# Kernel tuning notes

Hardware: AMD Instinct MI355X
Metric: run time of the kernel (lower is better)

Reference implementation:

```python
import jax, jax.numpy as jnp
from jax import lax
import numpy as np

NUM_BLOCK, NUM_LAYER = 4, 10
DILATIONS = [2 ** (i % NUM_LAYER) for i in range(NUM_BLOCK * NUM_LAYER)]


def setup_inputs() -> dict:
    key = jax.random.key(0)
    ks = jax.random.split(key, 6)
    s = 0.05
    return {
        "x": jax.random.normal(ks[0], (8, 256, 16000), dtype=jnp.float32),
        "W_start": jax.random.normal(ks[1], (32, 256), dtype=jnp.float32) * s,
        "W_dil": jax.random.normal(ks[2], (40, 128, 32, 2), dtype=jnp.float32) * s,
        "W_res": jax.random.normal(ks[3], (40, 32, 128), dtype=jnp.float32) * s,
        "W_e1": jax.random.normal(ks[4], (256, 32), dtype=jnp.float32) * s,
        "W_e2": jax.random.normal(ks[5], (256, 256), dtype=jnp.float32) * s,
    }


def _causal_dilated_conv(x, w, dilation):
    # x: [B, Cin, T], w: [Cout, Cin, K=2]. Left-pad (K-1)*dilation -> causal,
    # equivalent to torch symmetric-pad-then-trim-right.
    pad = (w.shape[-1] - 1) * dilation
    return lax.conv_general_dilated(
        x, w, window_strides=(1,), padding=[(pad, 0)],
        rhs_dilation=(dilation,), dimension_numbers=("NCH", "OIH", "NCH"))


def reference(x, W_start, W_dil, W_res, W_e1, W_e2):
    # start 1x1 conv (no bias)
    residual = jnp.einsum("oc,bct->bot", W_start, x)  # [B,32,T]
    skips = jnp.zeros_like(residual)
    for i, d in enumerate(DILATIONS):
        h = _causal_dilated_conv(residual, W_dil[i], d)       # [B,128,T]
        g = jnp.tanh(h) * jax.nn.sigmoid(h)                   # gated activation
        skip = jnp.einsum("oc,bct->bot", W_res[i], g)         # 1x1 -> [B,32,T]
        residual = residual + skip
        skips = skips + skip
    h = jax.nn.relu(skips)
    h = jax.nn.relu(jnp.einsum("oc,bct->bot", W_e1, h))       # [B,256,T]
    logits = jnp.einsum("oc,bct->bot", W_e2, h)               # [B,256,T]
    return logits
```

## Files before the change

### kernel.cpp

```cpp
#include <hip/hip_runtime.h>
#include <math.h>

#define T_LEN 16000
#define NTILE 250
#define TT 64
#define NBLK 2000
#define LGRID 500

static const int N_RES = 8 * 32 * T_LEN;

typedef _Float16 half_t;
typedef __attribute__((ext_vector_type(8))) _Float16 halfx8;
typedef __attribute__((ext_vector_type(4))) _Float16 halfx4;
typedef __attribute__((ext_vector_type(16))) float f32x16;
typedef unsigned int uint32;
typedef unsigned short ushort16;

#define MFMA(a, b, c) __builtin_amdgcn_mfma_f32_32x32x16_f16((a), (b), (c), 0, 0, 0)

static __device__ inline uint32 packpair(float a, float b) {
  half_t ha = (half_t)a, hb = (half_t)b;
  return (uint32)__builtin_bit_cast(ushort16, ha) |
         ((uint32)__builtin_bit_cast(ushort16, hb) << 16);
}

__global__ __launch_bounds__(256) void repack_k(
    const float* __restrict__ Wd, const float* __restrict__ Wr,
    const float* __restrict__ Ws, const float* __restrict__ We1,
    const float* __restrict__ We2,
    half_t* __restrict__ WaG, half_t* __restrict__ WrG, half_t* __restrict__ WsS,
    half_t* __restrict__ We1S, half_t* __restrict__ We2S) {
  int i = blockIdx.x * 256 + threadIdx.x;
  if (i < 40 * 128 * 128) {
    int l = i >> 14, r = i & 16383, o = r >> 7, k = r & 127;
    int kk = k & 63, c = kk >> 1, s = kk & 1;
    float w = Wd[(((l * 128 + o) * 32 + c) << 1) + s];
    half_t w0 = (half_t)w;
    WaG[i] = (k < 64) ? w0 : (half_t)((w - (float)w0) * 2048.f);
  }
  if (i < 40 * 32 * 256) {
    int l = i >> 13, r = i & 8191, o2 = r >> 8, k = r & 255;
    int kk = k & 127;
    int ks = kk >> 4, lh = (kk >> 3) & 1, j = kk & 7;
    int mh = ks >> 2, til = (ks >> 1) & 1, ab = ks & 1;
    int m = mh * 64 + til * 32 + ab * 16 + (j & 3) + ((j >> 2) << 3) + lh * 4;
    float w = Wr[(l * 32 + o2) * 128 + m];
    half_t w0 = (half_t)w;
    WrG[i] = (k < 128) ? w0 : (half_t)((w - (float)w0) * 2048.f);
  }
  if (i < 16384) {
    int o = i >> 9, k = i & 511, kk = k & 255;
    int chan = (kk >> 1) + (kk & 1) * 128;
    float w = Ws[o * 256 + chan];
    half_t w0 = (half_t)w;
    WsS[i] = (k < 256) ? w0 : (half_t)((w - (float)w0) * 2048.f);
  }
  if (i < 16384) {
    int o = i >> 6, k = i & 63;
    float w = We1[o * 32 + (k & 31)];
    half_t w0 = (half_t)w;
    We1S[i] = (k < 32) ? w0 : (half_t)((w - (float)w0) * 2048.f);
  }
  if (i < 131072) {
    int o = i >> 9, k = i & 511;
    float w = We2[o * 256 + (k & 255)];
    half_t w0 = (half_t)w;
    We2S[i] = (k < 256) ? w0 : (half_t)((w - (float)w0) * 2048.f);
  }
}

__global__ __launch_bounds__(256, 2) void start_k(const float* __restrict__ x,
                                                  const half_t* __restrict__ WsS,
                                                  float* __restrict__ res) {
  __shared__ __align__(16) char sm[51200];
  const int XS_OFF = 0, SKB_OFF = 33792;
  int tid = threadIdx.x;
  int wave = tid >> 6, lane = tid & 63;
  int l31 = lane & 31, lhi = lane >> 5;
  int nh = wave & 1, kh = wave >> 1;
  int b = blockIdx.x / NTILE;
  int t0 = (blockIdx.x % NTILE) * TT;
  int cth = tid >> 3, twh = (tid & 7) * 8;

  f32x16 accH{}, accL{};
#pragma unroll
  for (int p = 0; p < 2; ++p) {
#pragma unroll
    for (int cc = 0; cc < 4; ++cc) {
      const float* p0 = x + ((size_t)b * 256 + cc * 32 + cth) * T_LEN + t0 + twh;
      const float* p1 = p0 + (size_t)128 * T_LEN;
      float u[8], v[8];
      *(float4*)u       = *(const float4*)p0;
      *(float4*)(u + 4) = *(const float4*)(p0 + 4);
      *(float4*)v       = *(const float4*)p1;
      *(float4*)(v + 4) = *(const float4*)(p1 + 4);
#pragma unroll
      for (int j = 0; j < 8; ++j) {
        int t = twh + j;
        int sw = ((t >> 3) & 3) << 5;
        uint32 pk;
        if (p == 0) {
          pk = packpair(u[j], v[j]);
        } else {
          float l0 = (u[j] - (float)(half_t)u[j]) * 2048.f;
          float l1 = (v[j] - (float)(half_t)v[j]) * 2048.f;
          pk = packpair(l0, l1);
        }
        *(uint32*)(sm + XS_OFF + t * 528 + (((cc * 32 + cth) * 4) ^ sw)) = pk;
      }
    }
    __syncthreads();
    {
      int colt = nh * 32 + l31;
      int sw = ((colt >> 3) & 3) << 5;
      const char* xr = sm + XS_OFF + colt * 528;
#pragma unroll
      for (int ks = 0; ks < 8; ++ks) {
        int kg = kh * 8 + ks;
        halfx8 bf = *(const halfx8*)(xr + ((kg * 32 + lhi * 16) ^ sw));
        halfx8 hiA = *(const halfx8*)(WsS + l31 * 512 + kg * 16 + lhi * 8);
        if (p == 0) {
          accH = MFMA(hiA, bf, accH);
          halfx8 loA = *(const halfx8*)(WsS + l31 * 512 + 256 + kg * 16 + lhi * 8);
          accL = MFMA(loA, bf, accL);
        } else {
          accL = MFMA(hiA, bf, accL);
        }
      }
    }
    __syncthreads();
  }
  {
    float* skb = (float*)(sm + SKB_OFF) + kh * 32 * 68;
#pragma unroll
    for (int r = 0; r < 16; ++r) {
      int row = (r & 3) + 8 * (r >> 2) + 4 * lhi;
      skb[row * 68 + nh * 32 + l31] = accH[r] + accL[r] * (1.f / 2048.f);
    }
  }
  __syncthreads();
  {
    const float* s0 = (const float*)(sm + SKB_OFF) + cth * 68 + twh;
    const float* s1 = s0 + 32 * 68;
    float* rp = res + ((size_t)b * 32 + cth) * T_LEN + t0 + twh;
#pragma unroll
    for (int vq = 0; vq < 8; vq += 4) {
      float4 sa = *(const float4*)(s0 + vq);
      float4 sb = *(const float4*)(s1 + vq);
      float4 o;
      o.x = sa.x + sb.x;
      o.y = sa.y + sb.y;
      o.z = sa.z + sb.z;
      o.w = sa.w + sb.w;
      *(float4*)(rp + vq) = o;
    }
  }
}

#define LOAD_TILE(TI, CV, PV)                                              \
  {                                                                        \
    int tl_ = blockIdx.x + (TI) * LGRID;                                   \
    int bb_ = tl_ / NTILE;                                                 \
    int tb_ = (tl_ - bb_ * NTILE) * TT;                                    \
    const float* rip_ = resIn + ((size_t)bb_ * 32 + cth) * T_LEN;          \
    *(float4*)(CV)       = *(const float4*)(rip_ + tb_ + twh);             \
    *(float4*)((CV) + 4) = *(const float4*)(rip_ + tb_ + twh + 4);         \
    int tp_ = tb_ + twh - d;                                               \
    if (tp_ >= 0 && (d & 3) == 0) {                                        \
      *(float4*)(PV)       = *(const float4*)(rip_ + tp_);                 \
      *(float4*)((PV) + 4) = *(const float4*)(rip_ + tp_ + 4);             \
    } else {                                                               \
      _Pragma("unroll")                                                    \
      for (int j_ = 0; j_ < 8; ++j_) {                                     \
        int q_ = tp_ + j_;                                                 \
        (PV)[j_] = (q_ >= 0) ? rip_[q_] : 0.f;                             \
      }                                                                    \
    }                                                                      \
  }

#define STAGE_TILE(CV, PV)                                                 \
  {                                                                        \
    _Pragma("unroll")                                                      \
    for (int j = 0; j < 8; ++j) {                                          \
      int t = twh + j;                                                     \
      int sw = ((t >> 3) & 3) << 5;                                        \
      char* zrow = sm + t * 272;                                           \
      half_t p0 = (half_t)(PV)[j];                                         \
      half_t c0 = (half_t)(CV)[j];                                         \
      float pl = ((PV)[j] - (float)p0) * 2048.f;                           \
      float cl = ((CV)[j] - (float)c0) * 2048.f;                           \
      *(uint32*)(zrow + ((cth * 4) ^ sw))       = packpair((PV)[j], (CV)[j]); \
      *(uint32*)(zrow + ((cth * 4 + 128) ^ sw)) = packpair(pl, cl);        \
    }                                                                      \
  }

#define TILE_BODY(TI, CV, PV, NCV, NPV, PREF)                                  \
  {                                                                            \
    int tile = blockIdx.x + (TI) * LGRID;                                      \
    int b = tile / NTILE;                                                      \
    int t0 = (tile - b * NTILE) * TT;                                          \
    if (PREF) { LOAD_TILE((TI) + 1, NCV, NPV); }                               \
                                      \
    f32x16 hi0{}, hi1{}, lo0{}, lo1{};                                         \
    {                                                                          \
      int colt = nh * 32 + l31;                                                \
      int sw = ((colt >> 3) & 3) << 5;                                         \
      const char* zr = sm + colt * 272;                                        \
      _Pragma("unroll")                                                        \
      for (int ks = 0; ks < 12; ++ks) {                                        \
        int brow = (ks < 4) ? ks * 16                                          \
                            : ((ks < 8) ? (ks & 3) * 16 + 64 : (ks & 3) * 16); \
        halfx8 bf = *(const halfx8*)(zr + ((brow * 2 + lhi * 16) ^ sw));       \
        if (ks < 4) {                                                          \
          hi0 = MFMA(a1h0[ks], bf, hi0);                                       \
          hi1 = MFMA(a1h1[ks], bf, hi1);                                       \
        } else if (ks < 8) {                                                   \
          lo0 = MFMA(a1h0[ks & 3], bf, lo0);                                   \
          lo1 = MFMA(a1h1[ks & 3], bf, lo1);                                   \
        } else {                                                               \
          lo0 = MFMA(a1l0[ks & 3], bf, lo0);                                   \
          lo1 = MFMA(a1l1[ks & 3], bf, lo1);                                   \
        }                                                                      \
      }                                                                        \
    }                                                                          \
                          \
    halfx8 gh0a, gh0b, gl0a, gl0b, gh1a, gh1b, gl1a, gl1b;                     \
    _Pragma("unroll")                                                          \
    for (int r = 0; r < 16; ++r) {                                             \
      float ha = hi0[r] + lo0[r] * (1.f / 2048.f);                             \
      float hb = hi1[r] + lo1[r] * (1.f / 2048.f);                             \
      ha = fmaxf(ha, -30.f);                                                   \
      hb = fmaxf(hb, -30.f);                                                   \
      float ea = __expf(-ha), eb = __expf(-hb);                                \
      float ga = (1.f - ea) * __builtin_amdgcn_rcpf(1.f + ea * ea);            \
      float gb = (1.f - eb) * __builtin_amdgcn_rcpf(1.f + eb * eb);            \
      half_t ga0 = (half_t)ga;                                                 \
      half_t gb0 = (half_t)gb;                                                 \
      half_t ga1 = (half_t)((ga - (float)ga0) * 2048.f);                       \
      half_t gb1 = (half_t)((gb - (float)gb0) * 2048.f);                       \
      if (r < 8) {                                                             \
        gh0a[r] = ga0; gl0a[r] = ga1; gh1a[r] = gb0; gl1a[r] = gb1;            \
      } else {                                                                 \
        gh0b[r - 8] = ga0; gl0b[r - 8] = ga1;                                  \
        gh1b[r - 8] = gb0; gl1b[r - 8] = gb1;                                  \
      }                                                                        \
    }                                                                          \
                         \
    f32x16 shi{}, slo{};                                                       \
    shi = MFMA(wrHi[0], gh0a, shi);                                            \
    shi = MFMA(wrHi[1], gh0b, shi);                                            \
    shi = MFMA(wrHi[2], gh1a, shi);                                            \
    shi = MFMA(wrHi[3], gh1b, shi);                                            \
    slo = MFMA(wrHi[0], gl0a, slo);                                            \
    slo = MFMA(wrHi[1], gl0b, slo);                                            \
    slo = MFMA(wrHi[2], gl1a, slo);                                            \
    slo = MFMA(wrHi[3], gl1b, slo);                                            \
    slo = MFMA(wrLo[0], gh0a, slo);                                            \
    slo = MFMA(wrLo[1], gh0b, slo);                                            \
    slo = MFMA(wrLo[2], gh1a, slo);                                            \
    slo = MFMA(wrLo[3], gh1b, slo);                                            \
                                      \
    {                                                                          \
      float* skb = (float*)(sm + SKB_OFF) + mh * 32 * 68;                      \
      _Pragma("unroll")                                                        \
      for (int r = 0; r < 16; ++r) {                                           \
        int row = (r & 3) + 8 * (r >> 2) + 4 * lhi;                            \
        skb[row * 68 + nh * 32 + l31] = shi[r] + slo[r] * (1.f / 2048.f);      \
      }                                                                        \
    }                                                                          \
    __syncthreads();                                                           \
                 \
    {                                                                          \
      const float* s0 = (const float*)(sm + SKB_OFF) + cth * 68 + twh;         \
      const float* s1 = s0 + 32 * 68;                                          \
      size_t base = ((size_t)b * 32 + cth) * T_LEN + t0 + twh;                 \
      _Pragma("unroll")                                                        \
      for (int v = 0; v < 8; v += 4) {                                         \
        float4 sa = *(const float4*)(s0 + v);                                  \
        float4 sb = *(const float4*)(s1 + v);                                  \
        float4 o;                                                              \
        o.x = (CV)[v]     + sa.x + sb.x;                                       \
        o.y = (CV)[v + 1] + sa.y + sb.y;                                       \
        o.z = (CV)[v + 2] + sa.z + sb.z;                                       \
        o.w = (CV)[v + 3] + sa.w + sb.w;                                       \
        *(float4*)(resOut + base + v) = o;                                     \
      }                                                                        \
    }                                                                          \
    if (PREF) {                                                                \
      STAGE_TILE(NCV, NPV)                                                     \
      __syncthreads();                                                         \
    }                                                                          \
  }

__global__ __launch_bounds__(256, 2) void layer_k(const float* __restrict__ resIn,
                                                  float* __restrict__ resOut,
                                                  const half_t* __restrict__ WaL,
                                                  const half_t* __restrict__ WrL,
                                                  int d) {
  __shared__ __align__(16) char sm[34816];
  const int SKB_OFF = 17408;
  int tid = threadIdx.x;
  int wave = tid >> 6, lane = tid & 63;
  int l31 = lane & 31, lhi = lane >> 5;
  int mh = wave & 1, nh = wave >> 1;
  int cth = tid >> 3, twh = (tid & 7) * 8;

  halfx8 a1h0[4], a1l0[4], a1h1[4], a1l1[4];
  {
    const half_t* wa = WaL + (mh * 64 + l31) * 128 + lhi * 8;
#pragma unroll
    for (int j = 0; j < 4; ++j) {
      a1h0[j] = *(const halfx8*)(wa + j * 16);
      a1l0[j] = *(const halfx8*)(wa + 64 + j * 16);
      a1h1[j] = *(const halfx8*)(wa + 32 * 128 + j * 16);
      a1l1[j] = *(const halfx8*)(wa + 32 * 128 + 64 + j * 16);
    }
  }
  halfx8 wrHi[4], wrLo[4];
  {
    const half_t* wr = WrL + l31 * 256 + mh * 64 + lhi * 8;
#pragma unroll
    for (int q = 0; q < 4; ++q) {
      wrHi[q] = *(const halfx8*)(wr + q * 16);
      wrLo[q] = *(const halfx8*)(wr + 128 + q * 16);
    }
  }

  float cvA[8], pvA[8], cvB[8], pvB[8];
  LOAD_TILE(0, cvA, pvA);
  STAGE_TILE(cvA, pvA)
  __syncthreads();

  TILE_BODY(0, cvA, pvA, cvB, pvB, 1)
  TILE_BODY(1, cvB, pvB, cvA, pvA, 1)
  TILE_BODY(2, cvA, pvA, cvB, pvB, 1)
  TILE_BODY(3, cvB, pvB, cvA, pvA, 0)
}

__global__ __launch_bounds__(512, 6) void end_k(const float* __restrict__ resF,
                                                const float* __restrict__ res0,
                                                const half_t* __restrict__ We1S,
                                                const half_t* __restrict__ We2S,
                                                float* __restrict__ out) {
  __shared__ __align__(16) char sm[38912];
  const int H2T_OFF = 0, H1F_OFF = 0, H1T_OFF = 33792;
  int tid = threadIdx.x;
  int b = blockIdx.x / NTILE;
  int t0 = (blockIdx.x % NTILE) * TT;

  {
    int c = tid >> 4, tt4 = (tid & 15) * 4;
    size_t base = ((size_t)b * 32 + c) * T_LEN + t0 + tt4;
    float4 f = *(const float4*)(resF + base);
    float4 z = *(const float4*)(res0 + base);
    float* h1 = (float*)(sm + H1F_OFF) + c * 68 + tt4;
    h1[0] = fmaxf(f.x - z.x, 0.f);
    h1[1] = fmaxf(f.y - z.y, 0.f);
    h1[2] = fmaxf(f.z - z.z, 0.f);
    h1[3] = fmaxf(f.w - z.w, 0.f);
  }
  __syncthreads();
  {
    int t = tid & 63, cg2 = tid >> 6;
    const float* h1 = (const float*)(sm + H1F_OFF);
    halfx4 hi;
#pragma unroll
    for (int j = 0; j < 4; ++j) hi[j] = (half_t)h1[(cg2 * 4 + j) * 68 + t];
    *(halfx4*)(sm + H1T_OFF + t * 80 + cg2 * 8) = hi;
  }
  __syncthreads();

  int wave = tid >> 6, lane = tid & 63;
  int l31 = lane & 31, lhi = lane >> 5;

  f32x16 aHi0{}, aHi1{}, aLo0{}, aLo1{};
  {
    const char* h1t = sm + H1T_OFF;
    const half_t* wp = We1S + (wave * 32 + l31) * 64;
#pragma unroll
    for (int ks = 0; ks < 2; ++ks) {
      halfx8 hiA = *(const halfx8*)(wp + ks * 16 + lhi * 8);
      halfx8 loA = *(const halfx8*)(wp + 32 + ks * 16 + lhi * 8);
      halfx8 B0 = *(const halfx8*)(h1t + l31 * 80 + (ks * 16 + lhi * 8) * 2);
      halfx8 B1 = *(const halfx8*)(h1t + (32 + l31) * 80 + (ks * 16 + lhi * 8) * 2);
      aHi0 = MFMA(hiA, B0, aHi0);
      aLo0 = MFMA(loA, B0, aLo0);
      aHi1 = MFMA(hiA, B1, aHi1);
      aLo1 = MFMA(loA, B1, aLo1);
    }
  }
  {
#pragma unroll
    for (int n = 0; n < 2; ++n) {
      const f32x16& aH = n ? aHi1 : aHi0;
      const f32x16& aL = n ? aLo1 : aLo0;
      int t = n * 32 + l31;
      half_t* row = (half_t*)(sm + H2T_OFF) + t * 264;
#pragma unroll
      for (int g = 0; g < 4; ++g) {
        halfx4 hi;
#pragma unroll
        for (int j = 0; j < 4; ++j) {
          int r = g * 4 + j;
          float v = fmaxf(aH[r] + aL[r] * (1.f / 2048.f), 0.f);
          hi[j] = (half_t)v;
        }
        *(halfx4*)(row + wave * 32 + g * 8 + lhi * 4) = hi;
      }
    }
  }
  __syncthreads();

  f32x16 bHi0{}, bHi1{}, bLo0{}, bLo1{};
  {
    const half_t* wp = We2S + (size_t)(wave * 32 + l31) * 512;
    const char* h2t = sm + H2T_OFF;
#pragma unroll 2
    for (int ks = 0; ks < 16; ++ks) {
      halfx8 hiA = *(const halfx8*)(wp + ks * 16 + lhi * 8);
      halfx8 loA = *(const halfx8*)(wp + 256 + ks * 16 + lhi * 8);
      halfx8 B0 = *(const halfx8*)(h2t + l31 * 528 + (ks * 16 + lhi * 8) * 2);
      halfx8 B1 = *(const halfx8*)(h2t + (32 + l31) * 528 + (ks * 16 + lhi * 8) * 2);
      bHi0 = MFMA(hiA, B0, bHi0);
      bLo0 = MFMA(loA, B0, bLo0);
      bHi1 = MFMA(hiA, B1, bHi1);
      bLo1 = MFMA(loA, B1, bLo1);
    }
  }
  {
#pragma unroll
    for (int n = 0; n < 2; ++n) {
      const f32x16& bH = n ? bHi1 : bHi0;
      const f32x16& bL = n ? bLo1 : bLo0;
      int t = t0 + n * 32 + l31;
#pragma unroll
      for (int r = 0; r < 16; ++r) {
        int o = wave * 32 + (r & 3) + 8 * (r >> 2) + 4 * lhi;
        out[((size_t)b * 256 + o) * T_LEN + t] = bH[r] + bL[r] * (1.f / 2048.f);
      }
    }
  }
}

extern "C" void kernel_launch(void* const* d_in, const int* in_sizes, int n_in,
                              void* d_out, int out_size, void* d_ws, size_t ws_size,
                              hipStream_t stream) {
  const float* x   = (const float*)d_in[0];
  const float* Wst = (const float*)d_in[1];
  const float* Wd  = (const float*)d_in[2];
  const float* Wr  = (const float*)d_in[3];
  const float* We1 = (const float*)d_in[4];
  const float* We2 = (const float*)d_in[5];
  float* out = (float*)d_out;
  float* ws = (float*)d_ws;

  float* resA = ws;
  float* resB = resA + N_RES;
  float* resC = resB + N_RES;
  half_t* WaG  = (half_t*)(resC + N_RES);
  half_t* WrG  = WaG + 40 * 16384;
  half_t* WsS  = WrG + 40 * 8192;
  half_t* We1S = WsS + 16384;
  half_t* We2S = We1S + 16384;

  repack_k<<<2560, 256, 0, stream>>>(Wd, Wr, Wst, We1, We2, WaG, WrG, WsS, We1S, We2S);
  start_k<<<NBLK, 256, 0, stream>>>(x, WsS, resA);

  const float* rin = resA;
  for (int l = 0; l < 40; ++l) {
    float* rout = (l & 1) ? resC : resB;
    layer_k<<<LGRID, 256, 0, stream>>>(rin, rout, WaG + l * 16384, WrG + l * 8192,
                                       1 << (l % 10));
    rin = rout;
  }
  end_k<<<NBLK, 512, 0, stream>>>(rin, resA, We1S, We2S, out);
}
```

Measured before the change: 1.054 ms.

## Split layer kernel work across eight waves with quarter-channel ownership

The per-layer kernel moves from 256 to 512 threads. Each wave now owns 32 of the 128 dilated-conv output channels instead of 64, which halves the per-wave weight registers and accumulators. The residual-projection weights are repacked to match the quarter split, and the skip partial sums are reduced over four shared-memory slices instead of two. Each thread now loads and stages 4 timesteps instead of 8. The aim is more waves in flight to hide latency, at the cost of more shared memory per block and a wider cross-wave reduction.

Measured after the change: 1.066 ms. Within noise of the previous version (+1.1%).

```diff
diff --git a/kernel.cpp b/kernel.cpp
--- a/kernel.cpp
+++ b/kernel.cpp
@@ -41,9 +41,8 @@
   if (i < 40 * 32 * 256) {
     int l = i >> 13, r = i & 8191, o2 = r >> 8, k = r & 255;
     int kk = k & 127;
-    int ks = kk >> 4, lh = (kk >> 3) & 1, j = kk & 7;
-    int mh = ks >> 2, til = (ks >> 1) & 1, ab = ks & 1;
-    int m = mh * 64 + til * 32 + ab * 16 + (j & 3) + ((j >> 2) << 3) + lh * 4;
+    int mq = kk >> 5, ab = (kk >> 4) & 1, lh = (kk >> 3) & 1, j = kk & 7;
+    int m = mq * 32 + ab * 16 + lh * 4 + (j & 3) + ((j >> 2) << 3);
     float w = Wr[(l * 32 + o2) * 128 + m];
     half_t w0 = (half_t)w;
     WrG[i] = (k < 128) ? w0 : (half_t)((w - (float)w0) * 2048.f);
@@ -163,15 +162,13 @@
     int bb_ = tl_ / NTILE;                                                 \
     int tb_ = (tl_ - bb_ * NTILE) * TT;                                    \
     const float* rip_ = resIn + ((size_t)bb_ * 32 + cth) * T_LEN;          \
-    *(float4*)(CV)       = *(const float4*)(rip_ + tb_ + twh);             \
-    *(float4*)((CV) + 4) = *(const float4*)(rip_ + tb_ + twh + 4);         \
+    *(float4*)(CV) = *(const float4*)(rip_ + tb_ + twh);                   \
     int tp_ = tb_ + twh - d;                                               \
     if (tp_ >= 0 && (d & 3) == 0) {                                        \
-      *(float4*)(PV)       = *(const float4*)(rip_ + tp_);                 \
-      *(float4*)((PV) + 4) = *(const float4*)(rip_ + tp_ + 4);             \
+      *(float4*)(PV) = *(const float4*)(rip_ + tp_);                       \
     } else {                                                               \
       _Pragma("unroll")                                                    \
-      for (int j_ = 0; j_ < 8; ++j_) {                                     \
+      for (int j_ = 0; j_ < 4; ++j_) {                                     \
         int q_ = tp_ + j_;                                                 \
         (PV)[j_] = (q_ >= 0) ? rip_[q_] : 0.f;                             \
       }                                                                    \
@@ -181,7 +178,7 @@
 #define STAGE_TILE(CV, PV)                                                 \
   {                                                                        \
     _Pragma("unroll")                                                      \
-    for (int j = 0; j < 8; ++j) {                                          \
+    for (int j = 0; j < 4; ++j) {                                          \
       int t = twh + j;                                                     \
       int sw = ((t >> 3) & 3) << 5;                                        \
       char* zrow = sm + t * 272;                                           \
@@ -200,8 +197,8 @@
     int b = tile / NTILE;                                                      \
     int t0 = (tile - b * NTILE) * TT;                                          \
     if (PREF) { LOAD_TILE((TI) + 1, NCV, NPV); }                               \
-                                      \
-    f32x16 hi0{}, hi1{}, lo0{}, lo1{};                                         \
+                      \
+    f32x16 hi{}, lo{};                                                         \
     {                                                                          \
       int colt = nh * 32 + l31;                                                \
       int sw = ((colt >> 3) & 3) << 5;                                         \
@@ -211,57 +208,35 @@
         int brow = (ks < 4) ? ks * 16                                          \
                             : ((ks < 8) ? (ks & 3) * 16 + 64 : (ks & 3) * 16); \
         halfx8 bf = *(const halfx8*)(zr + ((brow * 2 + lhi * 16) ^ sw));       \
-        if (ks < 4) {                                                          \
-          hi0 = MFMA(a1h0[ks], bf, hi0);                                       \
-          hi1 = MFMA(a1h1[ks], bf, hi1);                                       \
-        } else if (ks < 8) {                                                   \
-          lo0 = MFMA(a1h0[ks & 3], bf, lo0);                                   \
-          lo1 = MFMA(a1h1[ks & 3], bf, lo1);                                   \
-        } else {                                                               \
-          lo0 = MFMA(a1l0[ks & 3], bf, lo0);                                   \
-          lo1 = MFMA(a1l1[ks & 3], bf, lo1);                                   \
-        }                                                                      \
+        if (ks < 4)      hi = MFMA(a1h[ks], bf, hi);                           \
+        else if (ks < 8) lo = MFMA(a1h[ks & 3], bf, lo);                       \
+        else             lo = MFMA(a1l[ks & 3], bf, lo);                       \
       }                                                                        \
     }                                                                          \
-                          \
-    halfx8 gh0a, gh0b, gl0a, gl0b, gh1a, gh1b, gl1a, gl1b;                     \
+                            \
+    halfx8 ghA, ghB, glA, glB;                                                 \
     _Pragma("unroll")                                                          \
     for (int r = 0; r < 16; ++r) {                                             \
-      float ha = hi0[r] + lo0[r] * (1.f / 2048.f);                             \
-      float hb = hi1[r] + lo1[r] * (1.f / 2048.f);                             \
+      float ha = hi[r] + lo[r] * (1.f / 2048.f);                               \
       ha = fmaxf(ha, -30.f);                                                   \
-      hb = fmaxf(hb, -30.f);                                                   \
-      float ea = __expf(-ha), eb = __expf(-hb);                                \
+      float ea = __expf(-ha);                                                  \
       float ga = (1.f - ea) * __builtin_amdgcn_rcpf(1.f + ea * ea);            \
-      float gb = (1.f - eb) * __builtin_amdgcn_rcpf(1.f + eb * eb);            \
       half_t ga0 = (half_t)ga;                                                 \
-      half_t gb0 = (half_t)gb;                                                 \
       half_t ga1 = (half_t)((ga - (float)ga0) * 2048.f);                       \
-      half_t gb1 = (half_t)((gb - (float)gb0) * 2048.f);                       \
-      if (r < 8) {                                                             \
-        gh0a[r] = ga0; gl0a[r] = ga1; gh1a[r] = gb0; gl1a[r] = gb1;            \
-      } else {                                                                 \
-        gh0b[r - 8] = ga0; gl0b[r - 8] = ga1;                                  \
-        gh1b[r - 8] = gb0; gl1b[r - 8] = gb1;                                  \
-      }                                                                        \
+      if (r < 8) { ghA[r] = ga0; glA[r] = ga1; }                               \
+      else       { ghB[r - 8] = ga0; glB[r - 8] = ga1; }                       \
     }                                                                          \
-                         \
+                 \
     f32x16 shi{}, slo{};                                                       \
-    shi = MFMA(wrHi[0], gh0a, shi);                                            \
-    shi = MFMA(wrHi[1], gh0b, shi);                                            \
-    shi = MFMA(wrHi[2], gh1a, shi);                                            \
-    shi = MFMA(wrHi[3], gh1b, shi);                                            \
-    slo = MFMA(wrHi[0], gl0a, slo);                                            \
-    slo = MFMA(wrHi[1], gl0b, slo);                                            \
-    slo = MFMA(wrHi[2], gl1a, slo);                                            \
-    slo = MFMA(wrHi[3], gl1b, slo);                                            \
-    slo = MFMA(wrLo[0], gh0a, slo);                                            \
-    slo = MFMA(wrLo[1], gh0b, slo);                                            \
-    slo = MFMA(wrLo[2], gh1a, slo);                                            \
-    slo = MFMA(wrLo[3], gh1b, slo);                                            \
-                                      \
+    shi = MFMA(wrHiA, ghA, shi);                                               \
+    shi = MFMA(wrHiB, ghB, shi);                                               \
+    slo = MFMA(wrHiA, glA, slo);                                               \
+    slo = MFMA(wrHiB, glB, slo);                                               \
+    slo = MFMA(wrLoA, ghA, slo);                                               \
+    slo = MFMA(wrLoB, ghB, slo);                                               \
+                                           \
     {                                                                          \
-      float* skb = (float*)(sm + SKB_OFF) + mh * 32 * 68;                      \
+      float* skb = (float*)(sm + SKB_OFF) + mq * 32 * 68;                      \
       _Pragma("unroll")                                                        \
       for (int r = 0; r < 16; ++r) {                                           \
         int row = (r & 3) + 8 * (r >> 2) + 4 * lhi;                            \
@@ -269,22 +244,20 @@
       }                                                                        \
     }                                                                          \
     __syncthreads();                                                           \
-                 \
+               \
     {                                                                          \
-      const float* s0 = (const float*)(sm + SKB_OFF) + cth * 68 + twh;         \
-      const float* s1 = s0 + 32 * 68;                                          \
+      const float* s = (const float*)(sm + SKB_OFF) + cth * 68 + twh;          \
+      float4 q0 = *(const float4*)s;                                           \
+      float4 q1 = *(const float4*)(s + 32 * 68);                               \
+      float4 q2 = *(const float4*)(s + 64 * 68);                               \
+      float4 q3 = *(const float4*)(s + 96 * 68);                               \
       size_t base = ((size_t)b * 32 + cth) * T_LEN + t0 + twh;                 \
-      _Pragma("unroll")                                                        \
-      for (int v = 0; v < 8; v += 4) {                                         \
-        float4 sa = *(const float4*)(s0 + v);                                  \
-        float4 sb = *(const float4*)(s1 + v);                                  \
-        float4 o;                                                              \
-        o.x = (CV)[v]     + sa.x + sb.x;                                       \
-        o.y = (CV)[v + 1] + sa.y + sb.y;                                       \
-        o.z = (CV)[v + 2] + sa.z + sb.z;                                       \
-        o.w = (CV)[v + 3] + sa.w + sb.w;                                       \
-        *(float4*)(resOut + base + v) = o;                                     \
-      }                                                                        \
+      float4 o;                                                                \
+      o.x = (CV)[0] + q0.x + q1.x + q2.x + q3.x;                               \
+      o.y = (CV)[1] + q0.y + q1.y + q2.y + q3.y;                               \
+      o.z = (CV)[2] + q0.z + q1.z + q2.z + q3.z;                               \
+      o.w = (CV)[3] + q0.w + q1.w + q2.w + q3.w;                               \
+      *(float4*)(resOut + base) = o;                                           \
     }                                                                          \
     if (PREF) {                                                                \
       STAGE_TILE(NCV, NPV)                                                     \
@@ -292,41 +265,38 @@
     }                                                                          \
   }
 
-__global__ __launch_bounds__(256, 2) void layer_k(const float* __restrict__ resIn,
+__global__ __launch_bounds__(512, 4) void layer_k(const float* __restrict__ resIn,
                                                   float* __restrict__ resOut,
                                                   const half_t* __restrict__ WaL,
                                                   const half_t* __restrict__ WrL,
                                                   int d) {
-  __shared__ __align__(16) char sm[34816];
+  __shared__ __align__(16) char sm[52224];
   const int SKB_OFF = 17408;
   int tid = threadIdx.x;
   int wave = tid >> 6, lane = tid & 63;
   int l31 = lane & 31, lhi = lane >> 5;
-  int mh = wave & 1, nh = wave >> 1;
-  int cth = tid >> 3, twh = (tid & 7) * 8;
-
-  halfx8 a1h0[4], a1l0[4], a1h1[4], a1l1[4];
-  {
-    const half_t* wa = WaL + (mh * 64 + l31) * 128 + lhi * 8;
+  int mq = wave & 3, nh = wave >> 2;
+  int cth = tid >> 4, twh = (tid & 15) * 4;
+
+  halfx8 a1h[4], a1l[4];
+  {
+    const half_t* wa = WaL + (mq * 32 + l31) * 128 + lhi * 8;
 #pragma unroll
     for (int j = 0; j < 4; ++j) {
-      a1h0[j] = *(const halfx8*)(wa + j * 16);
-      a1l0[j] = *(const halfx8*)(wa + 64 + j * 16);
-      a1h1[j] = *(const halfx8*)(wa + 32 * 128 + j * 16);
-      a1l1[j] = *(const halfx8*)(wa + 32 * 128 + 64 + j * 16);
-    }
-  }
-  halfx8 wrHi[4], wrLo[4];
-  {
-    const half_t* wr = WrL + l31 * 256 + mh * 64 + lhi * 8;
-#pragma unroll
-    for (int q = 0; q < 4; ++q) {
-      wrHi[q] = *(const halfx8*)(wr + q * 16);
-      wrLo[q] = *(const halfx8*)(wr + 128 + q * 16);
-    }
-  }
-
-  float cvA[8], pvA[8], cvB[8], pvB[8];
+      a1h[j] = *(const halfx8*)(wa + j * 16);
+      a1l[j] = *(const halfx8*)(wa + 64 + j * 16);
+    }
+  }
+  halfx8 wrHiA, wrHiB, wrLoA, wrLoB;
+  {
+    const half_t* wr = WrL + l31 * 256 + mq * 32 + lhi * 8;
+    wrHiA = *(const halfx8*)(wr);
+    wrHiB = *(const halfx8*)(wr + 16);
+    wrLoA = *(const halfx8*)(wr + 128);
+    wrLoB = *(const halfx8*)(wr + 144);
+  }
+
+  float cvA[4], pvA[4], cvB[4], pvB[4];
   LOAD_TILE(0, cvA, pvA);
   STAGE_TILE(cvA, pvA)
   __syncthreads();
@@ -469,7 +439,7 @@
   const float* rin = resA;
   for (int l = 0; l < 40; ++l) {
     float* rout = (l & 1) ? resC : resB;
-    layer_k<<<LGRID, 256, 0, stream>>>(rin, rout, WaG + l * 16384, WrG + l * 8192,
+    layer_k<<<LGRID, 512, 0, stream>>>(rin, rout, WaG + l * 16384, WrG + l * 8192,
                                        1 << (l % 10));
     rin = rout;
   }
```

## Double layer kernel tile width to 128 timesteps with 512-thread blocks

Applied to the files above, without the earlier changes.

Each layer_k block now handles 128-timestep tiles with 512 threads (8 waves), so each block covers two tiles instead of four and staging LDS doubles to about 67KB. The residual-projection weight fragments are reloaded inside each tile body rather than kept in registers for the whole kernel, freeing registers to fit the larger block under the launch bounds of (512,4). The aim is fewer sequential tile iterations per block and more waves in flight. The cost is heavier LDS use, which may cap occupancy, plus repeated weight loads.

New measurement: 1.954 ms. +85.3%, slower.

```diff
diff --git a/kernel.cpp b/kernel.cpp
--- a/kernel.cpp
+++ b/kernel.cpp
@@ -5,6 +5,7 @@
 #define NTILE 250
 #define TT 64
 #define NBLK 2000
+#define NT2 125
 #define LGRID 500
 
 static const int N_RES = 8 * 32 * T_LEN;
@@ -160,8 +161,8 @@
 #define LOAD_TILE(TI, CV, PV)                                              \
   {                                                                        \
     int tl_ = blockIdx.x + (TI) * LGRID;                                   \
-    int bb_ = tl_ / NTILE;                                                 \
-    int tb_ = (tl_ - bb_ * NTILE) * TT;                                    \
+    int bb_ = tl_ / NT2;                                                   \
+    int tb_ = (tl_ - bb_ * NT2) * 128;                                     \
     const float* rip_ = resIn + ((size_t)bb_ * 32 + cth) * T_LEN;          \
     *(float4*)(CV)       = *(const float4*)(rip_ + tb_ + twh);             \
     *(float4*)((CV) + 4) = *(const float4*)(rip_ + tb_ + twh + 4);         \
@@ -197,13 +198,13 @@
 #define TILE_BODY(TI, CV, PV, NCV, NPV, PREF)                                  \
   {                                                                            \
     int tile = blockIdx.x + (TI) * LGRID;                                      \
-    int b = tile / NTILE;                                                      \
-    int t0 = (tile - b * NTILE) * TT;                                          \
+    int b = tile / NT2;                                                        \
+    int t0 = (tile - b * NT2) * 128;                                           \
     if (PREF) { LOAD_TILE((TI) + 1, NCV, NPV); }                               \
-                                      \
+                      \
     f32x16 hi0{}, hi1{}, lo0{}, lo1{};                                         \
     {                                                                          \
-      int colt = nh * 32 + l31;                                                \
+      int colt = tq * 32 + l31;                                                \
       int sw = ((colt >> 3) & 3) << 5;                                         \
       const char* zr = sm + colt * 272;                                        \
       _Pragma("unroll")                                                        \
@@ -221,6 +222,16 @@
           lo0 = MFMA(a1l0[ks & 3], bf, lo0);                                   \
           lo1 = MFMA(a1l1[ks & 3], bf, lo1);                                   \
         }                                                                      \
+      }                                                                        \
+    }                                                                          \
+                    \
+    halfx8 wrHi[4], wrLo[4];                                                   \
+    {                                                                          \
+      const half_t* wr = WrL + l31 * 256 + mh * 64 + lhi * 8;                  \
+      _Pragma("unroll")                                                        \
+      for (int q = 0; q < 4; ++q) {                                            \
+        wrHi[q] = *(const halfx8*)(wr + q * 16);                               \
+        wrLo[q] = *(const halfx8*)(wr + 128 + q * 16);                         \
       }                                                                        \
     }                                                                          \
                           \
@@ -245,7 +256,7 @@
         gh1b[r - 8] = gb0; gl1b[r - 8] = gb1;                                  \
       }                                                                        \
     }                                                                          \
-                         \
+            \
     f32x16 shi{}, slo{};                                                       \
     shi = MFMA(wrHi[0], gh0a, shi);                                            \
     shi = MFMA(wrHi[1], gh0b, shi);                                            \
@@ -259,20 +270,20 @@
     slo = MFMA(wrLo[1], gh0b, slo);                                            \
     slo = MFMA(wrLo[2], gh1a, slo);                                            \
     slo = MFMA(wrLo[3], gh1b, slo);                                            \
-                                      \
+                                                   \
     {                                                                          \
-      float* skb = (float*)(sm + SKB_OFF) + mh * 32 * 68;                      \
+      float* skb = (float*)(sm + SKB_OFF) + mh * 32 * 132;                     \
       _Pragma("unroll")                                                        \
       for (int r = 0; r < 16; ++r) {                                           \
         int row = (r & 3) + 8 * (r >> 2) + 4 * lhi;                            \
-        skb[row * 68 + nh * 32 + l31] = shi[r] + slo[r] * (1.f / 2048.f);      \
+        skb[row * 132 + tq * 32 + l31] = shi[r] + slo[r] * (1.f / 2048.f);     \
       }                                                                        \
     }                                                                          \
     __syncthreads();                                                           \
                  \
     {                                                                          \
-      const float* s0 = (const float*)(sm + SKB_OFF) + cth * 68 + twh;         \
-      const float* s1 = s0 + 32 * 68;                                          \
+      const float* s0 = (const float*)(sm + SKB_OFF) + cth * 132 + twh;        \
+      const float* s1 = s0 + 32 * 132;                                         \
       size_t base = ((size_t)b * 32 + cth) * T_LEN + t0 + twh;                 \
       _Pragma("unroll")                                                        \
       for (int v = 0; v < 8; v += 4) {                                         \
@@ -292,18 +303,18 @@
     }                                                                          \
   }
 
-__global__ __launch_bounds__(256, 2) void layer_k(const float* __restrict__ resIn,
+__global__ __launch_bounds__(512, 4) void layer_k(const float* __restrict__ resIn,
                                                   float* __restrict__ resOut,
                                                   const half_t* __restrict__ WaL,
                                                   const half_t* __restrict__ WrL,
                                                   int d) {
-  __shared__ __align__(16) char sm[34816];
-  const int SKB_OFF = 17408;
+  __shared__ __align__(16) char sm[68608];
+  const int SKB_OFF = 34816;
   int tid = threadIdx.x;
   int wave = tid >> 6, lane = tid & 63;
   int l31 = lane & 31, lhi = lane >> 5;
-  int mh = wave & 1, nh = wave >> 1;
-  int cth = tid >> 3, twh = (tid & 7) * 8;
+  int mh = wave & 1, tq = wave >> 1;
+  int cth = tid >> 4, twh = (tid & 15) * 8;
 
   halfx8 a1h0[4], a1l0[4], a1h1[4], a1l1[4];
   {
@@ -316,15 +327,6 @@
       a1l1[j] = *(const halfx8*)(wa + 32 * 128 + 64 + j * 16);
     }
   }
-  halfx8 wrHi[4], wrLo[4];
-  {
-    const half_t* wr = WrL + l31 * 256 + mh * 64 + lhi * 8;
-#pragma unroll
-    for (int q = 0; q < 4; ++q) {
-      wrHi[q] = *(const halfx8*)(wr + q * 16);
-      wrLo[q] = *(const halfx8*)(wr + 128 + q * 16);
-    }
-  }
 
   float cvA[8], pvA[8], cvB[8], pvB[8];
   LOAD_TILE(0, cvA, pvA);
@@ -332,9 +334,7 @@
   __syncthreads();
 
   TILE_BODY(0, cvA, pvA, cvB, pvB, 1)
-  TILE_BODY(1, cvB, pvB, cvA, pvA, 1)
-  TILE_BODY(2, cvA, pvA, cvB, pvB, 1)
-  TILE_BODY(3, cvB, pvB, cvA, pvA, 0)
+  TILE_BODY(1, cvB, pvB, cvA, pvA, 0)
 }
 
 __global__ __launch_bounds__(512, 6) void end_k(const float* __restrict__ resF,
@@ -469,7 +469,7 @@
   const float* rin = resA;
   for (int l = 0; l < 40; ++l) {
     float* rout = (l & 1) ? resC : resB;
-    layer_k<<<LGRID, 256, 0, stream>>>(rin, rout, WaG + l * 16384, WrG + l * 8192,
+    layer_k<<<LGRID, 512, 0, stream>>>(rin, rout, WaG + l * 16384, WrG + l * 8192,
                                        1 << (l % 10));
     rin = rout;
   }
```
